# Performance work log

Hardware: AMD Instinct MI355X
Metric: run time of the kernel (lower is better)

## Reference

```python
import jax, jax.numpy as jnp
import numpy as np

B, I, T, H, O = 256, 128, 256, 512, 2
EPS = 1e-5  # BatchNorm1d default eps


def setup_inputs() -> dict:
    key = jax.random.key(0)
    ks = jax.random.split(key, 32)
    stdv = 1.0 / np.sqrt(H)
    u = lambda k, shape: jax.random.uniform(k, shape, jnp.float32, -stdv, stdv)
    X = jax.random.normal(ks[0], (B, I, T), jnp.float32)
    Mask = (jax.random.uniform(ks[1], (B, I, T)) > 0.5).astype(jnp.float32)
    Delta = jax.random.uniform(ks[2], (B, I, T)) * 5.0
    inp = jnp.stack([X, Mask, Delta], axis=1)  # [B, 3, I, T]
    return dict(
        input=inp,
        x_mean=jnp.float32(0.0),
        W_dg_x=u(ks[3], (I, I)), b_dg_x=u(ks[4], (I,)),
        W_dg_h=u(ks[5], (I, H)), b_dg_h=u(ks[6], (H,)),
        W_xz=u(ks[7], (I, H)), W_hz=u(ks[8], (H, H)), W_mz=u(ks[9], (I, H)), b_z=u(ks[10], (H,)),
        W_xr=u(ks[11], (I, H)), W_hr=u(ks[12], (H, H)), W_mr=u(ks[13], (I, H)), b_r=u(ks[14], (H,)),
        W_xh=u(ks[15], (I, H)), W_hh=u(ks[16], (H, H)), W_mh=u(ks[17], (I, H)), b_h=u(ks[18], (H,)),
        W_hy=u(ks[19], (H, O)), b_hy=u(ks[20], (O,)),
        bn_gamma=u(ks[21], (H,)), bn_beta=u(ks[22], (H,)),
    )


def reference(input, x_mean, W_dg_x, b_dg_x, W_dg_h, b_dg_h,
              W_xz, W_hz, W_mz, b_z, W_xr, W_hr, W_mr, b_r,
              W_xh, W_hh, W_mh, b_h, W_hy, b_hy, bn_gamma, bn_beta):
    # input: [B, 3, I, T] -> time-major [T, B, I]
    Xs = jnp.transpose(input[:, 0], (2, 0, 1))
    Ms = jnp.transpose(input[:, 1], (2, 0, 1))
    Ds = jnp.transpose(input[:, 2], (2, 0, 1))
    b, i = input.shape[0], input.shape[2]
    h0 = jnp.zeros((b, W_hz.shape[0]), input.dtype)       # Hidden_State buffer (zeros, broadcast over batch)
    xl0 = jnp.zeros((b, i), input.dtype)                   # X_last_obs buffer

    def step(carry, xs):
        h, x_last = carry
        x, m, d = xs
        gamma_x = jnp.exp(-jax.nn.relu(d @ W_dg_x + b_dg_x))   # [B, I]
        gamma_h = jnp.exp(-jax.nn.relu(d @ W_dg_h + b_dg_h))   # [B, H]
        x_last = jnp.where(m > 0, x, x_last)
        x = m * x + (1 - m) * (gamma_x * x_last + (1 - gamma_x) * x_mean)
        h = gamma_h * h
        z = jax.nn.sigmoid(x @ W_xz + h @ W_hz + m @ W_mz + b_z)
        r = jax.nn.sigmoid(x @ W_xr + h @ W_hr + m @ W_mr + b_r)
        h_tilde = jnp.tanh(x @ W_xh + (r * h) @ W_hh + m @ W_mh + b_h)
        h = (1 - z) * h + z * h_tilde
        # BatchNorm1d in training mode: batch mean, biased variance
        mu = h.mean(axis=0)
        var = ((h - mu) ** 2).mean(axis=0)
        h = bn_gamma * (h - mu) * jax.lax.rsqrt(var + EPS) + bn_beta
        y = jax.nn.softplus(h @ W_hy + b_hy)
        return (h, x_last), (y, h)

    _, (ys, hs) = jax.lax.scan(step, (h0, xl0), (Xs, Ms, Ds))
    # back to batch-major [B, T, *]
    return jnp.transpose(ys, (1, 0, 2)), jnp.transpose(hs, (1, 0, 2))
```

## Files before the change

kernel.cpp:

```cpp
#include <hip/hip_runtime.h>
#include <math.h>

#define Bb 256
#define Ii 128
#define Tt 256
#define Hh 512
#define Oo 2
#define TBr (Tt*Bb)
#define EPS_BN 1e-5f

typedef __attribute__((ext_vector_type(8))) short short8;
typedef __attribute__((ext_vector_type(8))) __bf16 bf16x8;
typedef __attribute__((ext_vector_type(4))) float f32x4;
typedef __attribute__((ext_vector_type(2))) float f32x2;
typedef unsigned long long u64;

__device__ __forceinline__ f32x4 mfma_bf16(short8 a, short8 b, f32x4 c) {
    return __builtin_amdgcn_mfma_f32_16x16x32_bf16(
        __builtin_bit_cast(bf16x8, a), __builtin_bit_cast(bf16x8, b), c, 0, 0, 0);
}
__device__ __forceinline__ short f2bf(float f) {
    union { float f; unsigned u; } v; v.f = f;
    unsigned r = (v.u + 0x7FFFu + ((v.u >> 16) & 1u)) >> 16;
    return (short)r;
}
__device__ __forceinline__ float bf2f(short s) {
    union { unsigned u; float f; } v; v.u = ((unsigned)(unsigned short)s) << 16;
    return v.f;
}
__device__ __forceinline__ float sigmoidf_(float x) { return 1.f / (1.f + expf(-x)); }
__device__ __forceinline__ float softplusf_(float x) { return fmaxf(x, 0.f) + log1pf(expf(-fabsf(x))); }

#define ALD_F(p)  __hip_atomic_load((p),  __ATOMIC_RELAXED, __HIP_MEMORY_SCOPE_AGENT)
#define AST_F(p,v) __hip_atomic_store((p), (v), __ATOMIC_RELAXED, __HIP_MEMORY_SCOPE_AGENT)
#define AADD_F(p,v) (void)__hip_atomic_fetch_add((p), (v), __ATOMIC_RELAXED, __HIP_MEMORY_SCOPE_AGENT)

__global__ __launch_bounds__(1024) void repack_kernel(const float* __restrict__ in,
                                                      float* __restrict__ Xall,
                                                      short* __restrict__ Mall,
                                                      short* __restrict__ Dall)
{
    __shared__ float tile[32][33];
    const int bz = blockIdx.z;
    const int b = bz / 3, cch = bz % 3;
    const int t0 = blockIdx.x * 32, i0 = blockIdx.y * 32;
    const int tx = threadIdx.x, ty = threadIdx.y;
    const float* src = in + ((size_t)b * 3 + cch) * (size_t)Ii * Tt;
    tile[ty][tx] = src[(size_t)(i0 + ty) * Tt + t0 + tx];
    __syncthreads();
    const float v = tile[tx][ty];
    const size_t off = ((size_t)(t0 + ty) * Bb + b) * Ii + i0 + tx;
    if (cch == 0)      Xall[off] = v;
    else if (cch == 1) Mall[off] = f2bf(v);
    else               Dall[off] = f2bf(v);
}

__global__ __launch_bounds__(256) void pack_weights_kernel(
    const float* __restrict__ W_dg_x, const float* __restrict__ W_dg_h,
    const float* __restrict__ W_xz, const float* __restrict__ W_hz, const float* __restrict__ W_mz, const float* __restrict__ b_z,
    const float* __restrict__ W_xr, const float* __restrict__ W_hr, const float* __restrict__ W_mr, const float* __restrict__ b_r,
    const float* __restrict__ W_xh, const float* __restrict__ W_hh, const float* __restrict__ W_mh,
    short* __restrict__ Wc1T, short* __restrict__ Wc2T,
    short* __restrict__ WdgxT, short* __restrict__ WdghT, float* __restrict__ bias1)
{
    const int idx = blockIdx.x * blockDim.x + threadIdx.x;
    const int n1 = 1024 * 768, n2 = 512 * 768, n3 = 128 * 128, n4 = 512 * 128;
    if (idx < n1) {
        const int n = idx / 768, k = idx % 768;
        const int col = (n < Hh) ? n : (n - Hh);
        const float* Wx = (n < Hh) ? W_xz : W_xr;
        const float* Wm = (n < Hh) ? W_mz : W_mr;
        const float* Wh = (n < Hh) ? W_hz : W_hr;
        float v;
        if (k < Ii)        v = Wx[(size_t)k * Hh + col];
        else if (k < 2*Ii) v = Wm[(size_t)(k - Ii) * Hh + col];
        else               v = Wh[(size_t)(k - 2*Ii) * Hh + col];
        Wc1T[idx] = f2bf(v);
    } else if (idx < n1 + n2) {
        const int j = idx - n1;
        const int n = j / 768, k = j % 768;
        float v;
        if (k < Ii)        v = W_xh[(size_t)k * Hh + n];
        else if (k < 2*Ii) v = W_mh[(size_t)(k - Ii) * Hh + n];
        else               v = W_hh[(size_t)(k - 2*Ii) * Hh + n];
        Wc2T[j] = f2bf(v);
    } else if (idx < n1 + n2 + n3) {
        const int j = idx - n1 - n2;
        const int n = j >> 7, k = j & 127;
        WdgxT[j] = f2bf(W_dg_x[(size_t)k * Ii + n]);
    } else if (idx < n1 + n2 + n3 + n4) {
        const int j = idx - n1 - n2 - n3;
        const int n = j >> 7, k = j & 127;
        WdghT[j] = f2bf(W_dg_h[(size_t)k * Hh + n]);
    } else if (idx < n1 + n2 + n3 + n4 + 1024) {
        const int n = idx - n1 - n2 - n3 - n4;
        bias1[n] = (n < Hh) ? b_z[n] : b_r[n - Hh];
    }
}

__global__ __launch_bounds__(64) void gdecay_kernel(const short* __restrict__ A,
                                                    const short* __restrict__ BT,
                                                    const float* __restrict__ bias,
                                                    short* __restrict__ C, int N)
{
    const int lane = threadIdx.x;
    const int c = lane & 15, g = lane >> 4;
    const int m0 = blockIdx.x * 32, n0 = blockIdx.y * 64;
    const short* a0 = A + (size_t)(m0 + c) * Ii + 8 * g;
    const short* a1 = a0 + (size_t)16 * Ii;
    const short* bw = BT + (size_t)(n0 + c) * Ii + 8 * g;
    f32x4 acc[2][4];
    #pragma unroll
    for (int i = 0; i < 2; ++i)
        #pragma unroll
        for (int f = 0; f < 4; ++f) acc[i][f] = (f32x4){0.f, 0.f, 0.f, 0.f};
    #pragma unroll
    for (int k0 = 0; k0 < 128; k0 += 32) {
        const short8 av0 = *(const short8*)(a0 + k0);
        const short8 av1 = *(const short8*)(a1 + k0);
        #pragma unroll
        for (int fn = 0; fn < 4; ++fn) {
            const short8 bv = *(const short8*)(bw + (size_t)fn * 16 * Ii + k0);
            acc[0][fn] = mfma_bf16(av0, bv, acc[0][fn]);
            acc[1][fn] = mfma_bf16(av1, bv, acc[1][fn]);
        }
    }
    #pragma unroll
    for (int fn = 0; fn < 4; ++fn) {
        const int n = n0 + fn * 16 + c;
        const float bs = bias[n];
        #pragma unroll
        for (int fm = 0; fm < 2; ++fm) {
            #pragma unroll
            for (int j = 0; j < 4; ++j) {
                const int m = m0 + fm * 16 + 4 * g + j;
                const float v = expf(-fmaxf(acc[fm][fn][j] + bs, 0.f));
                C[(size_t)m * N + n] = f2bf(v);
            }
        }
    }
}

__global__ __launch_bounds__(256) void xeff_scan_kernel(const float* __restrict__ Xall,
                                                        const short* __restrict__ Mall,
                                                        const short* __restrict__ Gx,
                                                        const float* __restrict__ xmean_p,
                                                        short* __restrict__ Xe)
{
    const int bi = blockIdx.x * blockDim.x + threadIdx.x;
    if (bi >= Bb * Ii) return;
    const float xm = xmean_p[0];
    float xl = 0.f;
    for (int t = 0; t < Tt; ++t) {
        const size_t off = (size_t)t * Bb * Ii + bi;
        const float x = Xall[off];
        const float m = bf2f(Mall[off]);
        const float gx = bf2f(Gx[off]);
        if (m > 0.f) xl = x;
        Xe[off] = f2bf(m * x + (1.f - m) * (gx * xl + (1.f - gx) * xm));
    }
}

#define XM_STR 264
#define HP_STR 520
#define RH_STR 520
#define GH_STR 520

__global__ __launch_bounds__(512, 1) void grud_persistent(
    const short* __restrict__ Xe, const short* __restrict__ Ma,
    const short* __restrict__ Ghb,
    const short* __restrict__ Wc1T, const short* __restrict__ Wc2T,
    const float* __restrict__ bias1, const float* __restrict__ b_h,
    const float* __restrict__ bn_g, const float* __restrict__ bn_b,
    const float* __restrict__ Why, const float* __restrict__ bhy,
    short* __restrict__ rhG,
    float* __restrict__ HrawG,
    float* __restrict__ PstSum,
    int* __restrict__ flags,
    float* __restrict__ out_hs, float* __restrict__ out_ys)
{
    const int bid = blockIdx.x, tid = threadIdx.x;
    const int w = tid >> 6, lane = tid & 63, c = lane & 15, g = lane >> 4;
    const int mt = bid & 15, ng = bid >> 4;
    const int m0 = mt * 16;

    __shared__ short sXM[16 * XM_STR];
    __shared__ short sHP[16 * HP_STR];
    __shared__ short sRH[16 * RH_STR];
    __shared__ short sGH[16 * GH_STR];
    __shared__ float sZ[32 * 17];
    __shared__ float scratch[1536];
    __shared__ float sWhy[1024];
    __shared__ float scs[512], shs[512];
    __shared__ float ysred[16];

    sWhy[tid] = Why[tid]; sWhy[tid + 512] = Why[tid + 512];
    const float bhy0 = bhy[0], bhy1 = bhy[1];

    const int colt = w & 3, kh = w >> 2;
    const int colbaseA = (colt < 2) ? (ng * 32 + colt * 16)
                                    : (512 + ng * 32 + (colt - 2) * 16);
    short8 wA[12];
    {
        const short* bw = Wc1T + (size_t)(colbaseA + c) * 768 + kh * 384 + 8 * g;
        #pragma unroll
        for (int s = 0; s < 12; ++s) wA[s] = *(const short8*)(bw + 32 * s);
    }
    const int colt2 = w & 1, kq = w >> 1;
    const int colbaseB = ng * 32 + colt2 * 16;
    short8 wB[6];
    {
        const short* bw = Wc2T + (size_t)(colbaseB + c) * 768 + kq * 192 + 8 * g;
        #pragma unroll
        for (int s = 0; s < 6; ++s) wB[s] = *(const short8*)(bw + 32 * s);
    }
    {
        const int r = tid >> 5, cu = tid & 31;
        const short* src = (cu < 16)
            ? (Xe + ((size_t)(m0 + r)) * Ii + 8 * cu)
            : (Ma + ((size_t)(m0 + r)) * Ii + 8 * (cu - 16));
        *(short8*)(&sXM[r * XM_STR + 8 * cu]) = *(const short8*)src;
    }
    __syncthreads();

    int ep = 0;
    for (int t = 0; t < Tt; ++t) {
        if (t > 0) {
            const int parP = (t - 1) & 1;
            {
                const float s1 = ALD_F(&PstSum[parP * 1024 + tid]);
                const float s2 = ALD_F(&PstSum[parP * 1024 + 512 + tid]);
                const float mu = s1 * (1.f / 256.f);
                const float var = fmaxf(s2 * (1.f / 256.f) - mu * mu, 0.f);
                const float sc = bn_g[tid] * rsqrtf(var + EPS_BN);
                scs[tid] = sc; shs[tid] = bn_b[tid] - mu * sc;
            }
            __syncthreads();
            float p0 = 0.f, p1 = 0.f;
            #pragma unroll
            for (int i = 0; i < 8; ++i) {
                const int idx = tid + i * 512;
                const int r = idx >> 8, c2 = (idx & 255) * 2;
                union { u64 u; float f[2]; } hv;
                hv.u = ALD_F((const u64*)(HrawG + (size_t)(m0 + r) * Hh + c2));
                const float h0 = fmaf(hv.f[0], scs[c2],     shs[c2]);
                const float h1 = fmaf(hv.f[1], scs[c2 + 1], shs[c2 + 1]);
                const unsigned gv = *(const unsigned*)(&sGH[r * GH_STR + c2]);
                const unsigned pk = (unsigned)(unsigned short)f2bf(h0 * bf2f((short)(gv & 0xffffu)))
                                  | ((unsigned)(unsigned short)f2bf(h1 * bf2f((short)(gv >> 16))) << 16);
                *(unsigned*)(&sHP[r * HP_STR + c2]) = pk;
                if ((c2 >> 5) == ng) {
                    *(f32x2*)(&out_hs[((size_t)(m0 + r) * Tt + (t - 1)) * Hh + c2]) = (f32x2){h0, h1};
                }
                if (r == ng) {
                    p0 = fmaf(h0, sWhy[2 * c2],     fmaf(h1, sWhy[2 * c2 + 2], p0));
                    p1 = fmaf(h0, sWhy[2 * c2 + 1], fmaf(h1, sWhy[2 * c2 + 3], p1));
                }
            }
            #pragma unroll
            for (int s = 1; s < 64; s <<= 1) { p0 += __shfl_xor(p0, s); p1 += __shfl_xor(p1, s); }
            if (lane == 0) { ysred[2 * w] = p0; ysred[2 * w + 1] = p1; }
            __syncthreads();
            if (tid == 0) {
                float q0 = 0.f, q1 = 0.f;
                #pragma unroll
                for (int i = 0; i < 8; ++i) { q0 += ysred[2 * i]; q1 += ysred[2 * i + 1]; }
                out_ys[((size_t)(m0 + ng) * Tt + (t - 1)) * Oo + 0] = softplusf_(q0 + bhy0);
                out_ys[((size_t)(m0 + ng) * Tt + (t - 1)) * Oo + 1] = softplusf_(q1 + bhy1);
            }
        } else {
            #pragma unroll
            for (int i = 0; i < 4; ++i) {
                const int e = tid + i * 512;
                const int r = e >> 7, cu = e & 127;
                *(u64*)(&sHP[r * HP_STR + 4 * cu]) = 0ull;
            }
            __syncthreads();
        }

        {
            f32x4 acc = (f32x4){0.f, 0.f, 0.f, 0.f};
            #pragma unroll
            for (int s = 0; s < 12; ++s) {
                const int k = kh * 384 + 32 * s;
                const short8 frag = (k < 256)
                    ? *(const short8*)(&sXM[c * XM_STR + k + 8 * g])
                    : *(const short8*)(&sHP[c * HP_STR + (k - 256) + 8 * g]);
                acc = mfma_bf16(wA[s], frag, acc);
            }
            if (kh == 1) {
                float* sp = scratch + (colt * 64 + lane) * 4;
                sp[0] = acc[0]; sp[1] = acc[1]; sp[2] = acc[2]; sp[3] = acc[3];
            }
            __syncthreads();
            if (kh == 0) {
                const float* sp = scratch + (colt * 64 + lane) * 4;
                acc[0] += sp[0]; acc[1] += sp[1]; acc[2] += sp[2]; acc[3] += sp[3];
                if (colt < 2) {
                    #pragma unroll
                    for (int j = 0; j < 4; ++j) {
                        const int lc = colt * 16 + 4 * g + j;
                        const float v = sigmoidf_(acc[j] + bias1[ng * 32 + lc]);
                        sZ[lc * 17 + c] = v;
                    }
                } else {
                    const int nn0 = ng * 32 + (colt - 2) * 16 + 4 * g;
                    short rh[4];
                    #pragma unroll
                    for (int j = 0; j < 4; ++j) {
                        const float v = sigmoidf_(acc[j] + bias1[512 + nn0 + j]);
                        rh[j] = f2bf(v * bf2f(sHP[c * HP_STR + nn0 + j]));
                    }
                    AST_F((u64*)(rhG + ((size_t)(m0 + c) * Hh + nn0)), *(const u64*)rh);
                }
            }
        }
        ep += 1;
        __syncthreads();
        if (tid == 0) AST_F(&flags[bid * 16], ep);
        if (t + 1 < Tt) {
            #pragma unroll
            for (int i = 0; i < 4; ++i) {
                const int e = tid + i * 512;
                const int r = e >> 7, c4 = e & 127;
                const u64 v = *(const u64*)(Ghb + ((size_t)(t + 1) * Bb + m0 + r) * Hh + 4 * c4);
                *(u64*)(&sGH[r * GH_STR + 4 * c4]) = v;
            }
        }
        if (tid < 256) {
            while (__hip_atomic_load(&flags[tid * 16], __ATOMIC_RELAXED, __HIP_MEMORY_SCOPE_AGENT) < ep)
                __builtin_amdgcn_s_sleep(1);
        }
        __syncthreads();

        #pragma unroll
        for (int i = 0; i < 4; ++i) {
            const int e = tid + i * 512;
            const int r = e >> 7, cu = e & 127;
            const u64 v = ALD_F((const u64*)(rhG + ((size_t)(m0 + r) * Hh + 4 * cu)));
            *(u64*)(&sRH[r * RH_STR + 4 * cu]) = v;
        }
        if (tid < 4) AST_F(&PstSum[((t + 1) & 1) * 1024 + bid * 4 + tid], 0.f);
        __syncthreads();

        {
            f32x4 acc2 = (f32x4){0.f, 0.f, 0.f, 0.f};
            #pragma unroll
            for (int s = 0; s < 6; ++s) {
                const int k = kq * 192 + 32 * s;
                const short8 frag = (k < 256)
                    ? *(const short8*)(&sXM[c * XM_STR + k + 8 * g])
                    : *(const short8*)(&sRH[c * RH_STR + (k - 256) + 8 * g]);
                acc2 = mfma_bf16(wB[s], frag, acc2);
            }
            if (kq > 0) {
                float* sp = scratch + ((colt2 * 3 + kq - 1) * 64 + lane) * 4;
                sp[0] = acc2[0]; sp[1] = acc2[1]; sp[2] = acc2[2]; sp[3] = acc2[3];
            }
            __syncthreads();
            if (kq == 0) {
                #pragma unroll
                for (int qq = 0; qq < 3; ++qq) {
                    const float* sp = scratch + ((colt2 * 3 + qq) * 64 + lane) * 4;
                    acc2[0] += sp[0]; acc2[1] += sp[1]; acc2[2] += sp[2]; acc2[3] += sp[3];
                }
                const int parC = t & 1;
                float hr4[4];
                #pragma unroll
                for (int j = 0; j < 4; ++j) {
                    const int lc = colt2 * 16 + 4 * g + j;
                    const int col = ng * 32 + lc;
                    const float pre = acc2[j] + b_h[col];
                    const float z = sZ[lc * 17 + c];
                    const float hp = bf2f(sHP[c * HP_STR + col]);
                    const float hr = (1.f - z) * hp + z * tanhf(pre);
                    hr4[j] = hr;
                    float sp_ = hr, sq_ = hr * hr;
                    sp_ += __shfl_xor(sp_, 1); sq_ += __shfl_xor(sq_, 1);
                    sp_ += __shfl_xor(sp_, 2); sq_ += __shfl_xor(sq_, 2);
                    sp_ += __shfl_xor(sp_, 4); sq_ += __shfl_xor(sq_, 4);
                    sp_ += __shfl_xor(sp_, 8); sq_ += __shfl_xor(sq_, 8);
                    if (c == 0) {
                        AADD_F(&PstSum[parC * 1024 + col], sp_);
                        AADD_F(&PstSum[parC * 1024 + 512 + col], sq_);
                    }
                }
                const int cb = ng * 32 + colt2 * 16 + 4 * g;
                AST_F((u64*)(HrawG + (size_t)(m0 + c) * Hh + cb),     *(const u64*)&hr4[0]);
                AST_F((u64*)(HrawG + (size_t)(m0 + c) * Hh + cb + 2), *(const u64*)&hr4[2]);
            }
        }
        ep += 1;
        __syncthreads();
        if (tid == 0) AST_F(&flags[bid * 16], ep);
        if (t + 1 < Tt) {
            const int r = tid >> 5, cu = tid & 31;
            const short* src = (cu < 16)
                ? (Xe + ((size_t)(t + 1) * Bb + m0 + r) * Ii + 8 * cu)
                : (Ma + ((size_t)(t + 1) * Bb + m0 + r) * Ii + 8 * (cu - 16));
            *(short8*)(&sXM[r * XM_STR + 8 * cu]) = *(const short8*)src;
        }
        if (tid < 256) {
            while (__hip_atomic_load(&flags[tid * 16], __ATOMIC_RELAXED, __HIP_MEMORY_SCOPE_AGENT) < ep)
                __builtin_amdgcn_s_sleep(1);
        }
        __syncthreads();
    }

    {
        const int parP = (Tt - 1) & 1;
        {
            const float s1 = ALD_F(&PstSum[parP * 1024 + tid]);
            const float s2 = ALD_F(&PstSum[parP * 1024 + 512 + tid]);
            const float mu = s1 * (1.f / 256.f);
            const float var = fmaxf(s2 * (1.f / 256.f) - mu * mu, 0.f);
            const float sc = bn_g[tid] * rsqrtf(var + EPS_BN);
            scs[tid] = sc; shs[tid] = bn_b[tid] - mu * sc;
        }
        __syncthreads();
        float p0 = 0.f, p1 = 0.f;
        #pragma unroll
        for (int i = 0; i < 8; ++i) {
            const int idx = tid + i * 512;
            const int r = idx >> 8, c2 = (idx & 255) * 2;
            union { u64 u; float f[2]; } hv;
            hv.u = ALD_F((const u64*)(HrawG + (size_t)(m0 + r) * Hh + c2));
            const float h0 = fmaf(hv.f[0], scs[c2],     shs[c2]);
            const float h1 = fmaf(hv.f[1], scs[c2 + 1], shs[c2 + 1]);
            if ((c2 >> 5) == ng) {
                *(f32x2*)(&out_hs[((size_t)(m0 + r) * Tt + (Tt - 1)) * Hh + c2]) = (f32x2){h0, h1};
            }
            if (r == ng) {
                p0 = fmaf(h0, sWhy[2 * c2],     fmaf(h1, sWhy[2 * c2 + 2], p0));
                p1 = fmaf(h0, sWhy[2 * c2 + 1], fmaf(h1, sWhy[2 * c2 + 3], p1));
            }
        }
        #pragma unroll
        for (int s = 1; s < 64; s <<= 1) { p0 += __shfl_xor(p0, s); p1 += __shfl_xor(p1, s); }
        if (lane == 0) { ysred[2 * w] = p0; ysred[2 * w + 1] = p1; }
        __syncthreads();
        if (tid == 0) {
            float q0 = 0.f, q1 = 0.f;
            #pragma unroll
            for (int i = 0; i < 8; ++i) { q0 += ysred[2 * i]; q1 += ysred[2 * i + 1]; }
            out_ys[((size_t)(m0 + ng) * Tt + (Tt - 1)) * Oo + 0] = softplusf_(q0 + bhy0);
            out_ys[((size_t)(m0 + ng) * Tt + (Tt - 1)) * Oo + 1] = softplusf_(q1 + bhy1);
        }
    }
}

extern "C" void kernel_launch(void* const* d_in, const int* in_sizes, int n_in,
                              void* d_out, int out_size, void* d_ws, size_t ws_size,
                              hipStream_t stream)
{
    const float* input  = (const float*)d_in[0];
    const float* xmean  = (const float*)d_in[1];
    const float* W_dg_x = (const float*)d_in[2];
    const float* b_dg_x = (const float*)d_in[3];
    const float* W_dg_h = (const float*)d_in[4];
    const float* b_dg_h = (const float*)d_in[5];
    const float* W_xz   = (const float*)d_in[6];
    const float* W_hz   = (const float*)d_in[7];
    const float* W_mz   = (const float*)d_in[8];
    const float* b_z    = (const float*)d_in[9];
    const float* W_xr   = (const float*)d_in[10];
    const float* W_hr   = (const float*)d_in[11];
    const float* W_mr   = (const float*)d_in[12];
    const float* b_r    = (const float*)d_in[13];
    const float* W_xh   = (const float*)d_in[14];
    const float* W_hh   = (const float*)d_in[15];
    const float* W_mh   = (const float*)d_in[16];
    const float* b_h    = (const float*)d_in[17];
    const float* W_hy   = (const float*)d_in[18];
    const float* b_hy   = (const float*)d_in[19];
    const float* bn_g   = (const float*)d_in[20];
    const float* bn_b   = (const float*)d_in[21];

    float* out_ys = (float*)d_out;
    float* out_hs = out_ys + (size_t)Bb * Tt * Oo;

    char* p = (char*)d_ws;
    float* Xall = (float*)p;            p += (size_t)TBr * Ii * 4;
    short* Mall = (short*)p;            p += (size_t)TBr * Ii * 2;
    short* Dall = (short*)p;            p += (size_t)TBr * Ii * 2;
    short* Gxb  = (short*)p;            p += (size_t)TBr * Ii * 2;
    short* Ghb  = (short*)p;            p += (size_t)TBr * Hh * 2;
    short* Xe   = (short*)p;            p += (size_t)TBr * Ii * 2;
    short* Wc1T = (short*)p;            p += (size_t)1024 * 768 * 2;
    short* Wc2T = (short*)p;            p += (size_t)512 * 768 * 2;
    short* WdgxT= (short*)p;            p += (size_t)128 * 128 * 2;
    short* WdghT= (short*)p;            p += (size_t)512 * 128 * 2;
    float* bias1= (float*)p;            p += 1024 * 4;
    short* rhG  = (short*)p;            p += (size_t)Bb * Hh * 2;
    float* HrawG= (float*)p;            p += (size_t)Bb * Hh * 4;
    float* PstSum=(float*)p;            p += 2 * 1024 * 4;
    int*   flags= (int*)p;              p += 256 * 16 * 4;

    hipMemsetAsync(flags, 0, 256 * 16 * 4, stream);
    hipMemsetAsync(PstSum, 0, 2 * 1024 * 4, stream);

    repack_kernel<<<dim3(Tt / 32, Ii / 32, Bb * 3), dim3(32, 32), 0, stream>>>(input, Xall, Mall, Dall);

    {
        const int total = 1024 * 768 + 512 * 768 + 128 * 128 + 512 * 128 + 1024;
        pack_weights_kernel<<<(total + 255) / 256, 256, 0, stream>>>(
            W_dg_x, W_dg_h,
            W_xz, W_hz, W_mz, b_z,
            W_xr, W_hr, W_mr, b_r,
            W_xh, W_hh, W_mh,
            Wc1T, Wc2T, WdgxT, WdghT, bias1);
    }

    gdecay_kernel<<<dim3(TBr / 32, Ii / 64), 64, 0, stream>>>(Dall, WdgxT, b_dg_x, Gxb, Ii);
    gdecay_kernel<<<dim3(TBr / 32, Hh / 64), 64, 0, stream>>>(Dall, WdghT, b_dg_h, Ghb, Hh);

    xeff_scan_kernel<<<(Bb * Ii) / 256, 256, 0, stream>>>(Xall, Mall, Gxb, xmean, Xe);

    grud_persistent<<<256, 512, 0, stream>>>(
        Xe, Mall, Ghb, Wc1T, Wc2T, bias1, b_h, bn_g, bn_b,
        W_hy, b_hy, rhG, HrawG, PstSum, flags, out_hs, out_ys);
}
```

Before: 2.728 ms.

## Narrow first barrier to same-row blocks, hoist input MFMAs, store hidden raw state as bf16

The first per-step grid barrier now waits only on the 16 blocks that share the same batch-row tile, since the r*h exchange is row-local. It does this through separate flag arrays and a three-slot BN statistics buffer, replacing the global wait on all 256 blocks. The MFMA contributions from x and mask are computed at the start of each step, before any waiting. r*h is read straight from global memory into the MFMA instead of being staged in LDS, and the raw hidden state is exchanged as bf16 to halve that traffic. In exchange the raw h carries bf16 rounding before BatchNorm, and the barrier logic becomes harder to get right.

```diff
diff --git a/kernel.cpp b/kernel.cpp
--- a/kernel.cpp
+++ b/kernel.cpp
@@ -34,6 +34,19 @@
 #define ALD_F(p)  __hip_atomic_load((p),  __ATOMIC_RELAXED, __HIP_MEMORY_SCOPE_AGENT)
 #define AST_F(p,v) __hip_atomic_store((p), (v), __ATOMIC_RELAXED, __HIP_MEMORY_SCOPE_AGENT)
 #define AADD_F(p,v) (void)__hip_atomic_fetch_add((p), (v), __ATOMIC_RELAXED, __HIP_MEMORY_SCOPE_AGENT)
+
+__device__ __forceinline__ short8 ald16(const short* p) {
+    union { u64 u[2]; short8 s; } v;
+    v.u[0] = ALD_F((const u64*)p);
+    v.u[1] = ALD_F((const u64*)(p + 4));
+    return v.s;
+}
+__device__ __forceinline__ u64 pack4bf(float a, float b, float c_, float d) {
+    return (u64)(unsigned short)f2bf(a)
+         | ((u64)(unsigned short)f2bf(b) << 16)
+         | ((u64)(unsigned short)f2bf(c_) << 32)
+         | ((u64)(unsigned short)f2bf(d) << 48);
+}
 
 __global__ __launch_bounds__(1024) void repack_kernel(const float* __restrict__ in,
                                                       float* __restrict__ Xall,
@@ -163,7 +176,6 @@
 
 #define XM_STR 264
 #define HP_STR 520
-#define RH_STR 520
 #define GH_STR 520
 
 __global__ __launch_bounds__(512, 1) void grud_persistent(
@@ -174,9 +186,10 @@
     const float* __restrict__ bn_g, const float* __restrict__ bn_b,
     const float* __restrict__ Why, const float* __restrict__ bhy,
     short* __restrict__ rhG,
-    float* __restrict__ HrawG,
+    short* __restrict__ HrawG,
     float* __restrict__ PstSum,
-    int* __restrict__ flags,
+    int* __restrict__ f1,
+    int* __restrict__ f2,
     float* __restrict__ out_hs, float* __restrict__ out_ys)
 {
     const int bid = blockIdx.x, tid = threadIdx.x;
@@ -186,7 +199,6 @@
 
     __shared__ short sXM[16 * XM_STR];
     __shared__ short sHP[16 * HP_STR];
-    __shared__ short sRH[16 * RH_STR];
     __shared__ short sGH[16 * GH_STR];
     __shared__ float sZ[32 * 17];
     __shared__ float scratch[1536];
@@ -223,13 +235,28 @@
     }
     __syncthreads();
 
-    int ep = 0;
     for (int t = 0; t < Tt; ++t) {
+        f32x4 accA = (f32x4){0.f, 0.f, 0.f, 0.f};
+        f32x4 accB = (f32x4){0.f, 0.f, 0.f, 0.f};
+        if (kh == 0) {
+            #pragma unroll
+            for (int s = 0; s < 8; ++s)
+                accA = mfma_bf16(wA[s],
+                    *(const short8*)(&sXM[c * XM_STR + 32 * s + 8 * g]), accA);
+        }
+        #pragma unroll
+        for (int s = 0; s < 6; ++s) {
+            const int k = kq * 192 + 32 * s;
+            if (k < 256)
+                accB = mfma_bf16(wB[s],
+                    *(const short8*)(&sXM[c * XM_STR + k + 8 * g]), accB);
+        }
+
         if (t > 0) {
-            const int parP = (t - 1) & 1;
+            const int pR = (t + 2) % 3;
             {
-                const float s1 = ALD_F(&PstSum[parP * 1024 + tid]);
-                const float s2 = ALD_F(&PstSum[parP * 1024 + 512 + tid]);
+                const float s1 = ALD_F(&PstSum[pR * 1024 + tid]);
+                const float s2 = ALD_F(&PstSum[pR * 1024 + 512 + tid]);
                 const float mu = s1 * (1.f / 256.f);
                 const float var = fmaxf(s2 * (1.f / 256.f) - mu * mu, 0.f);
                 const float sc = bn_g[tid] * rsqrtf(var + EPS_BN);
@@ -238,23 +265,29 @@
             __syncthreads();
             float p0 = 0.f, p1 = 0.f;
             #pragma unroll
-            for (int i = 0; i < 8; ++i) {
+            for (int i = 0; i < 4; ++i) {
                 const int idx = tid + i * 512;
-                const int r = idx >> 8, c2 = (idx & 255) * 2;
-                union { u64 u; float f[2]; } hv;
-                hv.u = ALD_F((const u64*)(HrawG + (size_t)(m0 + r) * Hh + c2));
-                const float h0 = fmaf(hv.f[0], scs[c2],     shs[c2]);
-                const float h1 = fmaf(hv.f[1], scs[c2 + 1], shs[c2 + 1]);
-                const unsigned gv = *(const unsigned*)(&sGH[r * GH_STR + c2]);
-                const unsigned pk = (unsigned)(unsigned short)f2bf(h0 * bf2f((short)(gv & 0xffffu)))
-                                  | ((unsigned)(unsigned short)f2bf(h1 * bf2f((short)(gv >> 16))) << 16);
-                *(unsigned*)(&sHP[r * HP_STR + c2]) = pk;
-                if ((c2 >> 5) == ng) {
-                    *(f32x2*)(&out_hs[((size_t)(m0 + r) * Tt + (t - 1)) * Hh + c2]) = (f32x2){h0, h1};
+                const int r = idx >> 7, c4 = (idx & 127) * 4;
+                union { u64 u; unsigned short us[4]; } hv, gv;
+                hv.u = ALD_F((const u64*)(HrawG + (size_t)(m0 + r) * Hh + c4));
+                gv.u = *(const u64*)(&sGH[r * GH_STR + c4]);
+                float h[4];
+                #pragma unroll
+                for (int j = 0; j < 4; ++j)
+                    h[j] = fmaf(bf2f((short)hv.us[j]), scs[c4 + j], shs[c4 + j]);
+                *(u64*)(&sHP[r * HP_STR + c4]) =
+                    pack4bf(h[0] * bf2f((short)gv.us[0]), h[1] * bf2f((short)gv.us[1]),
+                            h[2] * bf2f((short)gv.us[2]), h[3] * bf2f((short)gv.us[3]));
+                if ((c4 >> 5) == ng) {
+                    *(f32x4*)(&out_hs[((size_t)(m0 + r) * Tt + (t - 1)) * Hh + c4]) =
+                        (f32x4){h[0], h[1], h[2], h[3]};
                 }
                 if (r == ng) {
-                    p0 = fmaf(h0, sWhy[2 * c2],     fmaf(h1, sWhy[2 * c2 + 2], p0));
-                    p1 = fmaf(h0, sWhy[2 * c2 + 1], fmaf(h1, sWhy[2 * c2 + 3], p1));
+                    #pragma unroll
+                    for (int j = 0; j < 4; ++j) {
+                        p0 = fmaf(h[j], sWhy[2 * (c4 + j)], p0);
+                        p1 = fmaf(h[j], sWhy[2 * (c4 + j) + 1], p1);
+                    }
                 }
             }
             #pragma unroll
@@ -271,128 +304,115 @@
         } else {
             #pragma unroll
             for (int i = 0; i < 4; ++i) {
-                const int e = tid + i * 512;
-                const int r = e >> 7, cu = e & 127;
-                *(u64*)(&sHP[r * HP_STR + 4 * cu]) = 0ull;
+                const int idx = tid + i * 512;
+                const int r = idx >> 7, c4 = (idx & 127) * 4;
+                *(u64*)(&sHP[r * HP_STR + c4]) = 0ull;
             }
             __syncthreads();
         }
 
-        {
-            f32x4 acc = (f32x4){0.f, 0.f, 0.f, 0.f};
-            #pragma unroll
-            for (int s = 0; s < 12; ++s) {
-                const int k = kh * 384 + 32 * s;
-                const short8 frag = (k < 256)
-                    ? *(const short8*)(&sXM[c * XM_STR + k + 8 * g])
-                    : *(const short8*)(&sHP[c * HP_STR + (k - 256) + 8 * g]);
-                acc = mfma_bf16(wA[s], frag, acc);
-            }
-            if (kh == 1) {
-                float* sp = scratch + (colt * 64 + lane) * 4;
-                sp[0] = acc[0]; sp[1] = acc[1]; sp[2] = acc[2]; sp[3] = acc[3];
-            }
-            __syncthreads();
-            if (kh == 0) {
-                const float* sp = scratch + (colt * 64 + lane) * 4;
-                acc[0] += sp[0]; acc[1] += sp[1]; acc[2] += sp[2]; acc[3] += sp[3];
-                if (colt < 2) {
-                    #pragma unroll
-                    for (int j = 0; j < 4; ++j) {
-                        const int lc = colt * 16 + 4 * g + j;
-                        const float v = sigmoidf_(acc[j] + bias1[ng * 32 + lc]);
-                        sZ[lc * 17 + c] = v;
-                    }
-                } else {
-                    const int nn0 = ng * 32 + (colt - 2) * 16 + 4 * g;
-                    short rh[4];
-                    #pragma unroll
-                    for (int j = 0; j < 4; ++j) {
-                        const float v = sigmoidf_(acc[j] + bias1[512 + nn0 + j]);
-                        rh[j] = f2bf(v * bf2f(sHP[c * HP_STR + nn0 + j]));
-                    }
-                    AST_F((u64*)(rhG + ((size_t)(m0 + c) * Hh + nn0)), *(const u64*)rh);
-                }
-            }
-        }
-        ep += 1;
-        __syncthreads();
-        if (tid == 0) AST_F(&flags[bid * 16], ep);
-        if (t + 1 < Tt) {
-            #pragma unroll
-            for (int i = 0; i < 4; ++i) {
-                const int e = tid + i * 512;
-                const int r = e >> 7, c4 = e & 127;
-                const u64 v = *(const u64*)(Ghb + ((size_t)(t + 1) * Bb + m0 + r) * Hh + 4 * c4);
-                *(u64*)(&sGH[r * GH_STR + 4 * c4]) = v;
-            }
-        }
-        if (tid < 256) {
-            while (__hip_atomic_load(&flags[tid * 16], __ATOMIC_RELAXED, __HIP_MEMORY_SCOPE_AGENT) < ep)
-                __builtin_amdgcn_s_sleep(1);
-        }
-        __syncthreads();
-
-        #pragma unroll
-        for (int i = 0; i < 4; ++i) {
-            const int e = tid + i * 512;
-            const int r = e >> 7, cu = e & 127;
-            const u64 v = ALD_F((const u64*)(rhG + ((size_t)(m0 + r) * Hh + 4 * cu)));
-            *(u64*)(&sRH[r * RH_STR + 4 * cu]) = v;
-        }
-        if (tid < 4) AST_F(&PstSum[((t + 1) & 1) * 1024 + bid * 4 + tid], 0.f);
-        __syncthreads();
-
-        {
-            f32x4 acc2 = (f32x4){0.f, 0.f, 0.f, 0.f};
-            #pragma unroll
-            for (int s = 0; s < 6; ++s) {
-                const int k = kq * 192 + 32 * s;
-                const short8 frag = (k < 256)
-                    ? *(const short8*)(&sXM[c * XM_STR + k + 8 * g])
-                    : *(const short8*)(&sRH[c * RH_STR + (k - 256) + 8 * g]);
-                acc2 = mfma_bf16(wB[s], frag, acc2);
-            }
-            if (kq > 0) {
-                float* sp = scratch + ((colt2 * 3 + kq - 1) * 64 + lane) * 4;
-                sp[0] = acc2[0]; sp[1] = acc2[1]; sp[2] = acc2[2]; sp[3] = acc2[3];
-            }
-            __syncthreads();
-            if (kq == 0) {
-                #pragma unroll
-                for (int qq = 0; qq < 3; ++qq) {
-                    const float* sp = scratch + ((colt2 * 3 + qq) * 64 + lane) * 4;
-                    acc2[0] += sp[0]; acc2[1] += sp[1]; acc2[2] += sp[2]; acc2[3] += sp[3];
-                }
-                const int parC = t & 1;
-                float hr4[4];
+        if (kh == 0) {
+            #pragma unroll
+            for (int s = 8; s < 12; ++s)
+                accA = mfma_bf16(wA[s],
+                    *(const short8*)(&sHP[c * HP_STR + (32 * s - 256) + 8 * g]), accA);
+        } else {
+            #pragma unroll
+            for (int s = 0; s < 12; ++s)
+                accA = mfma_bf16(wA[s],
+                    *(const short8*)(&sHP[c * HP_STR + 128 + 32 * s + 8 * g]), accA);
+        }
+        if (kh == 1) {
+            float* sp = scratch + (colt * 64 + lane) * 4;
+            sp[0] = accA[0]; sp[1] = accA[1]; sp[2] = accA[2]; sp[3] = accA[3];
+        }
+        __syncthreads();
+        if (kh == 0) {
+            const float* sp = scratch + (colt * 64 + lane) * 4;
+            accA[0] += sp[0]; accA[1] += sp[1]; accA[2] += sp[2]; accA[3] += sp[3];
+            if (colt < 2) {
                 #pragma unroll
                 for (int j = 0; j < 4; ++j) {
-                    const int lc = colt2 * 16 + 4 * g + j;
-                    const int col = ng * 32 + lc;
-                    const float pre = acc2[j] + b_h[col];
-                    const float z = sZ[lc * 17 + c];
-                    const float hp = bf2f(sHP[c * HP_STR + col]);
-                    const float hr = (1.f - z) * hp + z * tanhf(pre);
-                    hr4[j] = hr;
-                    float sp_ = hr, sq_ = hr * hr;
-                    sp_ += __shfl_xor(sp_, 1); sq_ += __shfl_xor(sq_, 1);
-                    sp_ += __shfl_xor(sp_, 2); sq_ += __shfl_xor(sq_, 2);
-                    sp_ += __shfl_xor(sp_, 4); sq_ += __shfl_xor(sq_, 4);
-                    sp_ += __shfl_xor(sp_, 8); sq_ += __shfl_xor(sq_, 8);
-                    if (c == 0) {
-                        AADD_F(&PstSum[parC * 1024 + col], sp_);
-                        AADD_F(&PstSum[parC * 1024 + 512 + col], sq_);
-                    }
+                    const int lc = colt * 16 + 4 * g + j;
+                    const float v = sigmoidf_(accA[j] + bias1[ng * 32 + lc]);
+                    sZ[lc * 17 + c] = v;
                 }
-                const int cb = ng * 32 + colt2 * 16 + 4 * g;
-                AST_F((u64*)(HrawG + (size_t)(m0 + c) * Hh + cb),     *(const u64*)&hr4[0]);
-                AST_F((u64*)(HrawG + (size_t)(m0 + c) * Hh + cb + 2), *(const u64*)&hr4[2]);
-            }
-        }
-        ep += 1;
-        __syncthreads();
-        if (tid == 0) AST_F(&flags[bid * 16], ep);
+            } else {
+                const int nn0 = ng * 32 + (colt - 2) * 16 + 4 * g;
+                float rv[4];
+                #pragma unroll
+                for (int j = 0; j < 4; ++j) {
+                    const float v = sigmoidf_(accA[j] + bias1[512 + nn0 + j]);
+                    rv[j] = v * bf2f(sHP[c * HP_STR + nn0 + j]);
+                }
+                AST_F((u64*)(rhG + ((size_t)(m0 + c) * Hh + nn0)),
+                      pack4bf(rv[0], rv[1], rv[2], rv[3]));
+            }
+        }
+        __syncthreads();
+        if (tid == 0) AST_F(&f1[bid * 16], t + 1);
+        if (t + 1 < Tt) {
+            #pragma unroll
+            for (int i = 0; i < 4; ++i) {
+                const int idx = tid + i * 512;
+                const int r = idx >> 7, c4 = (idx & 127) * 4;
+                const u64 v = *(const u64*)(Ghb + ((size_t)(t + 1) * Bb + m0 + r) * Hh + c4);
+                *(u64*)(&sGH[r * GH_STR + c4]) = v;
+            }
+        }
+        if (tid < 4) AST_F(&PstSum[((t + 1) % 3) * 1024 + bid * 4 + tid], 0.f);
+        if (tid < 16) {
+            while (__hip_atomic_load(&f1[(mt + 16 * tid) * 16],
+                                     __ATOMIC_RELAXED, __HIP_MEMORY_SCOPE_AGENT) < t + 1)
+                __builtin_amdgcn_s_sleep(1);
+        }
+        __syncthreads();
+
+        #pragma unroll
+        for (int s = 0; s < 6; ++s) {
+            const int k = kq * 192 + 32 * s;
+            if (k >= 256)
+                accB = mfma_bf16(wB[s],
+                    ald16(rhG + (size_t)(m0 + c) * Hh + (k - 256) + 8 * g), accB);
+        }
+        if (kq > 0) {
+            float* sp = scratch + ((colt2 * 3 + kq - 1) * 64 + lane) * 4;
+            sp[0] = accB[0]; sp[1] = accB[1]; sp[2] = accB[2]; sp[3] = accB[3];
+        }
+        __syncthreads();
+        if (kq == 0) {
+            #pragma unroll
+            for (int qq = 0; qq < 3; ++qq) {
+                const float* sp = scratch + ((colt2 * 3 + qq) * 64 + lane) * 4;
+                accB[0] += sp[0]; accB[1] += sp[1]; accB[2] += sp[2]; accB[3] += sp[3];
+            }
+            const int pC = t % 3;
+            float hr4[4];
+            #pragma unroll
+            for (int j = 0; j < 4; ++j) {
+                const int lc = colt2 * 16 + 4 * g + j;
+                const int col = ng * 32 + lc;
+                const float pre = accB[j] + b_h[col];
+                const float z = sZ[lc * 17 + c];
+                const float hp = bf2f(sHP[c * HP_STR + col]);
+                const float hr = (1.f - z) * hp + z * tanhf(pre);
+                hr4[j] = hr;
+                float sp_ = hr, sq_ = hr * hr;
+                sp_ += __shfl_xor(sp_, 1); sq_ += __shfl_xor(sq_, 1);
+                sp_ += __shfl_xor(sp_, 2); sq_ += __shfl_xor(sq_, 2);
+                sp_ += __shfl_xor(sp_, 4); sq_ += __shfl_xor(sq_, 4);
+                sp_ += __shfl_xor(sp_, 8); sq_ += __shfl_xor(sq_, 8);
+                if (c == 0) {
+                    AADD_F(&PstSum[pC * 1024 + col], sp_);
+                    AADD_F(&PstSum[pC * 1024 + 512 + col], sq_);
+                }
+            }
+            const int cb = ng * 32 + colt2 * 16 + 4 * g;
+            AST_F((u64*)(HrawG + (size_t)(m0 + c) * Hh + cb),
+                  pack4bf(hr4[0], hr4[1], hr4[2], hr4[3]));
+        }
+        __syncthreads();
+        if (tid == 0) AST_F(&f2[bid * 16], t + 1);
         if (t + 1 < Tt) {
             const int r = tid >> 5, cu = tid & 31;
             const short* src = (cu < 16)
@@ -401,17 +421,18 @@
             *(short8*)(&sXM[r * XM_STR + 8 * cu]) = *(const short8*)src;
         }
         if (tid < 256) {
-            while (__hip_atomic_load(&flags[tid * 16], __ATOMIC_RELAXED, __HIP_MEMORY_SCOPE_AGENT) < ep)
+            while (__hip_atomic_load(&f2[tid * 16],
+                                     __ATOMIC_RELAXED, __HIP_MEMORY_SCOPE_AGENT) < t + 1)
                 __builtin_amdgcn_s_sleep(1);
         }
         __syncthreads();
     }
 
     {
-        const int parP = (Tt - 1) & 1;
+        const int pR = (Tt - 1) % 3;
         {
-            const float s1 = ALD_F(&PstSum[parP * 1024 + tid]);
-            const float s2 = ALD_F(&PstSum[parP * 1024 + 512 + tid]);
+            const float s1 = ALD_F(&PstSum[pR * 1024 + tid]);
+            const float s2 = ALD_F(&PstSum[pR * 1024 + 512 + tid]);
             const float mu = s1 * (1.f / 256.f);
             const float var = fmaxf(s2 * (1.f / 256.f) - mu * mu, 0.f);
             const float sc = bn_g[tid] * rsqrtf(var + EPS_BN);
@@ -420,19 +441,25 @@
         __syncthreads();
         float p0 = 0.f, p1 = 0.f;
         #pragma unroll
-        for (int i = 0; i < 8; ++i) {
+        for (int i = 0; i < 4; ++i) {
             const int idx = tid + i * 512;
-            const int r = idx >> 8, c2 = (idx & 255) * 2;
-            union { u64 u; float f[2]; } hv;
-            hv.u = ALD_F((const u64*)(HrawG + (size_t)(m0 + r) * Hh + c2));
-            const float h0 = fmaf(hv.f[0], scs[c2],     shs[c2]);
-            const float h1 = fmaf(hv.f[1], scs[c2 + 1], shs[c2 + 1]);
-            if ((c2 >> 5) == ng) {
-                *(f32x2*)(&out_hs[((size_t)(m0 + r) * Tt + (Tt - 1)) * Hh + c2]) = (f32x2){h0, h1};
+            const int r = idx >> 7, c4 = (idx & 127) * 4;
+            union { u64 u; unsigned short us[4]; } hv;
+            hv.u = ALD_F((const u64*)(HrawG + (size_t)(m0 + r) * Hh + c4));
+            float h[4];
+            #pragma unroll
+            for (int j = 0; j < 4; ++j)
+                h[j] = fmaf(bf2f((short)hv.us[j]), scs[c4 + j], shs[c4 + j]);
+            if ((c4 >> 5) == ng) {
+                *(f32x4*)(&out_hs[((size_t)(m0 + r) * Tt + (Tt - 1)) * Hh + c4]) =
+                    (f32x4){h[0], h[1], h[2], h[3]};
             }
             if (r == ng) {
-                p0 = fmaf(h0, sWhy[2 * c2],     fmaf(h1, sWhy[2 * c2 + 2], p0));
-                p1 = fmaf(h0, sWhy[2 * c2 + 1], fmaf(h1, sWhy[2 * c2 + 3], p1));
+                #pragma unroll
+                for (int j = 0; j < 4; ++j) {
+                    p0 = fmaf(h[j], sWhy[2 * (c4 + j)], p0);
+                    p1 = fmaf(h[j], sWhy[2 * (c4 + j) + 1], p1);
+                }
             }
         }
         #pragma unroll
@@ -492,12 +519,14 @@
     short* WdghT= (short*)p;            p += (size_t)512 * 128 * 2;
     float* bias1= (float*)p;            p += 1024 * 4;
     short* rhG  = (short*)p;            p += (size_t)Bb * Hh * 2;
-    float* HrawG= (float*)p;            p += (size_t)Bb * Hh * 4;
-    float* PstSum=(float*)p;            p += 2 * 1024 * 4;
-    int*   flags= (int*)p;              p += 256 * 16 * 4;
-
-    hipMemsetAsync(flags, 0, 256 * 16 * 4, stream);
-    hipMemsetAsync(PstSum, 0, 2 * 1024 * 4, stream);
+    short* HrawG= (short*)p;            p += (size_t)Bb * Hh * 2;
+    float* PstSum=(float*)p;            p += 3 * 1024 * 4;
+    int*   f1   = (int*)p;              p += 256 * 16 * 4;
+    int*   f2   = (int*)p;              p += 256 * 16 * 4;
+
+    hipMemsetAsync(f1, 0, 256 * 16 * 4, stream);
+    hipMemsetAsync(f2, 0, 256 * 16 * 4, stream);
+    hipMemsetAsync(PstSum, 0, 3 * 1024 * 4, stream);
 
     repack_kernel<<<dim3(Tt / 32, Ii / 32, Bb * 3), dim3(32, 32), 0, stream>>>(input, Xall, Mall, Dall);
 
@@ -518,5 +547,5 @@
 
     grud_persistent<<<256, 512, 0, stream>>>(
         Xe, Mall, Ghb, Wc1T, Wc2T, bias1, b_h, bn_g, bn_b,
-        W_hy, b_hy, rhG, HrawG, PstSum, flags, out_hs, out_ys);
-}
+        W_hy, b_hy, rhG, HrawG, PstSum, f1, f2, out_hs, out_ys);
+}
```

Result: no change. 2.681 ms (-1.7%).
